# Kernel tuning notes

Hardware: AMD Instinct MI355X
Metric: run time of the kernel (lower is better)

Reference implementation:

```python
import jax, jax.numpy as jnp
import numpy as np
import math

# l values of the spherical harmonics (mul=1 each), matching init_kwargs l=[0..8]
LS = [0, 1, 2, 3, 4, 5, 6, 7, 8]
LMAX = max(LS)
SQRT2 = math.sqrt(2.0)


def _legendre_coeffs(l, m):
    """Coefficients of the associated-Legendre polynomial used by e3nn:
    P_{l,m}(z,y) = norm * y^m * d^{l+m}/dz^{l+m} (z^2-1)^l,
    norm = sqrt((2l+1)/(4pi) (l-m)!/(l+m)!) / (2^l l!).
    Returns list of (power_of_z, float_coeff); the y^m factor is applied by the caller.
    Matches sympy expansion in _sympy_legendre/_poly_legendre exactly.
    """
    n = l + m
    norm = math.sqrt((2 * l + 1) / (4 * math.pi) * math.factorial(l - m) / math.factorial(l + m))
    norm /= (2.0 ** l) * math.factorial(l)
    out = []
    for k in range(l + 1):
        p = 2 * k  # (z^2-1)^l = sum_k C(l,k) (-1)^{l-k} z^{2k}
        if p >= n:
            c = math.comb(l, k) * ((-1) ** (l - k)) * (math.factorial(p) // math.factorial(p - n))
            out.append((p - n, norm * c))
    return out


def _powers(x, pmax):
    pows = [jnp.ones_like(x)]
    for _ in range(pmax):
        pows.append(pows[-1] * x)
    return pows  # pows[p] = x**p


def _legendre_eval(z, y):
    """Equivalent of the fx Legendre graph: [..., sum(2l+1)] with P_{l,|m|} repeated for m=-l..l."""
    zp = _powers(z, 2 * LMAX)
    yp = _powers(y, LMAX)
    cols = []
    for l in LS:
        legs = []
        for m in range(l + 1):
            acc = None
            for pw, c in _legendre_coeffs(l, m):
                term = c * zp[pw]
                acc = term if acc is None else acc + term
            legs.append(acc * yp[m])
        for m in range(-l, l + 1):
            cols.append(legs[abs(m)])
    return jnp.stack(cols, axis=-1)


def _sh_alpha(alpha):
    """spherical_harmonics_alpha for l=LMAX: [..., 2*LMAX+1]."""
    a = alpha[..., None]
    m = jnp.arange(1, LMAX + 1, dtype=alpha.dtype)
    cos = jnp.cos(m * a)           # m = 1..LMAX
    sin = jnp.sin(m[::-1] * a)     # m = LMAX..1
    return jnp.concatenate([SQRT2 * sin, jnp.ones_like(a), SQRT2 * cos], axis=-1)


def _mul_m_lm(x_m, x_lm):
    """Segment-wise multiply of [..., sum(2l+1)] by centered slices of [..., 2*LMAX+1]."""
    out = []
    i = 0
    for l in LS:
        d = 2 * l + 1
        out.append(x_lm[..., i:i + d] * x_m[..., LMAX - l:LMAX + l + 1])
        i += d
    return jnp.concatenate(out, axis=-1)


def setup_inputs() -> dict:
    key = jax.random.key(0)
    k1, k2 = jax.random.split(key)
    n = 1_048_576
    alpha = jax.random.uniform(k1, (n,), jnp.float32, 0.0, 2.0 * math.pi)
    beta = jax.random.uniform(k2, (n,), jnp.float32, 0.0, math.pi)
    return {"alpha": alpha, "beta": beta}


def reference(alpha, beta):
    # forward: y=cos(beta), z=sin(beta); Legendre graph placeholders are (z, y),
    # so the polynomial variable is cos(beta) and the y=sqrt(1-z^2) factor is sin(beta).
    z = jnp.cos(beta)
    y = jnp.sin(beta)
    sha = _sh_alpha(alpha.reshape(-1))                      # [N, 2*LMAX+1]
    shy = _legendre_eval(z.reshape(-1), y.reshape(-1))      # [N, sum(2l+1)]
    out = _mul_m_lm(sha, shy)
    return out.reshape(alpha.shape + (shy.shape[-1],))
```

## Files before the change

kernel.cpp:

```cpp
#include <hip/hip_runtime.h>

#define LMAXV 8
#define NCOL 81
#define ROWB 324
#define BLOCKSZ 64
#define BCHUNK (BLOCKSZ * ROWB)
#define NU4 (BCHUNK / 16)

typedef unsigned int u32x4 __attribute__((ext_vector_type(4)));

struct LMCoef { float c[5]; int T; int par; };

constexpr double cfact(int n) { double r = 1.0; for (int i = 2; i <= n; ++i) r *= (double)i; return r; }
constexpr double ccomb(int n, int k) { return cfact(n) / (cfact(k) * cfact(n - k)); }
constexpr double csqrt_(double x) { double g = x > 1.0 ? x : 1.0; for (int i = 0; i < 200; ++i) g = 0.5 * (g + x / g); return g; }
constexpr double CPI_ = 3.14159265358979323846;

constexpr LMCoef make_lm(int l, int m) {
  LMCoef r{{0.f, 0.f, 0.f, 0.f, 0.f}, 0, 0};
  const int n = l + m;
  const double norm = csqrt_((double)(2 * l + 1) / (4.0 * CPI_) * cfact(l - m) / cfact(l + m))
                      / ((double)(1 << l) * cfact(l));
  r.par = (l - m) & 1;
  r.T = (l - m) / 2 + 1;
  for (int j = 0; j < r.T; ++j) {
    const int p = 2 * j + r.par + n;
    const int k = p / 2;
    const double c = ccomb(l, k) * (((l - k) & 1) ? -1.0 : 1.0) * (cfact(p) / cfact(p - n));
    r.c[j] = (float)(norm * c);
  }
  return r;
}

constexpr LMCoef G_LM[45] = {
  make_lm(0,0),
  make_lm(1,0), make_lm(1,1),
  make_lm(2,0), make_lm(2,1), make_lm(2,2),
  make_lm(3,0), make_lm(3,1), make_lm(3,2), make_lm(3,3),
  make_lm(4,0), make_lm(4,1), make_lm(4,2), make_lm(4,3), make_lm(4,4),
  make_lm(5,0), make_lm(5,1), make_lm(5,2), make_lm(5,3), make_lm(5,4), make_lm(5,5),
  make_lm(6,0), make_lm(6,1), make_lm(6,2), make_lm(6,3), make_lm(6,4), make_lm(6,5), make_lm(6,6),
  make_lm(7,0), make_lm(7,1), make_lm(7,2), make_lm(7,3), make_lm(7,4), make_lm(7,5), make_lm(7,6), make_lm(7,7),
  make_lm(8,0), make_lm(8,1), make_lm(8,2), make_lm(8,3), make_lm(8,4), make_lm(8,5), make_lm(8,6), make_lm(8,7), make_lm(8,8)
};

__global__ __launch_bounds__(BLOCKSZ) void sh_ab_kernel(
    const float* __restrict__ alpha,
    const float* __restrict__ beta,
    float* __restrict__ out, int n)
{
  __shared__ u32x4 ldsbuf[NU4];
  float* lds = (float*)ldsbuf;

  const int tid = blockIdx.x * BLOCKSZ + threadIdx.x;

  float a = 0.f, b = 0.f;
  if (tid < n) {
    a = alpha[tid];
    b = beta[tid];
  }
  float sa, ca, sb, cbeta;
  __sincosf(a, &sa, &ca);
  __sincosf(b, &sb, &cbeta);
  const float z = cbeta, y = sb;
  const float z2 = z * z;

  float S[LMAXV + 1], C[LMAXV + 1];
  S[1] = 1.41421356237309505f * sa;
  C[1] = 1.41421356237309505f * ca;
#pragma unroll
  for (int m = 2; m <= LMAXV; ++m) {
    C[m] = C[m - 1] * ca - S[m - 1] * sa;
    S[m] = S[m - 1] * ca + C[m - 1] * sa;
  }

  float YM[LMAXV + 1], ZYM[LMAXV + 1];
  YM[0] = 1.f;
#pragma unroll
  for (int m = 1; m <= LMAXV; ++m) YM[m] = YM[m - 1] * y;
#pragma unroll
  for (int m = 0; m <= LMAXV; ++m) ZYM[m] = z * YM[m];

  float* myrow = lds + threadIdx.x * NCOL;

#pragma unroll
  for (int l = 0; l <= LMAXV; ++l) {
    float leg[LMAXV + 1];
#pragma unroll
    for (int mm = 0; mm <= l; ++mm) {
      const int idx = l * (l + 1) / 2 + mm;
      float v = 0.f;
#pragma unroll
      for (int j = 4; j >= 0; --j) {
        if (j < G_LM[idx].T) v = v * z2 + G_LM[idx].c[j];
      }
      leg[mm] = v * (G_LM[idx].par ? ZYM[mm] : YM[mm]);
    }
    const int colbase = l * l;
#pragma unroll
    for (int j = 0; j < l; ++j) {
      myrow[colbase + j] = leg[l - j] * S[l - j];
    }
    myrow[colbase + l] = leg[0];
#pragma unroll
    for (int j = 1; j <= l; ++j) {
      myrow[colbase + l + j] = leg[j] * C[j];
    }
  }

  __syncthreads();

  const u32x4* lsrc = (const u32x4*)lds;
  u32x4* gdst = (u32x4*)((char*)out + (size_t)blockIdx.x * BCHUNK);

  if (blockIdx.x != gridDim.x - 1) {
#pragma unroll
    for (int k = 0; k < 20; ++k) {
      const int o = threadIdx.x + (k << 6);
      gdst[o] = lsrc[o];
    }
    if (threadIdx.x < 16) {
      const int o = threadIdx.x + 1280;
      gdst[o] = lsrc[o];
    }
  } else {
    const long limitBytes = (long)n * ROWB - (long)blockIdx.x * BCHUNK;
    for (int o = threadIdx.x; o < NU4; o += BLOCKSZ) {
      if ((long)o * 16 < limitBytes) gdst[o] = lsrc[o];
    }
  }
}

extern "C" void kernel_launch(void* const* d_in, const int* in_sizes, int n_in,
                              void* d_out, int out_size, void* d_ws, size_t ws_size,
                              hipStream_t stream) {
  const float* alpha = (const float*)d_in[0];
  const float* beta  = (const float*)d_in[1];
  float* out = (float*)d_out;
  const int n = in_sizes[0];
  const int grid = (n + BLOCKSZ - 1) / BLOCKSZ;
  hipLaunchKernelGGL(sh_ab_kernel, dim3(grid), dim3(BLOCKSZ), 0, stream,
                     alpha, beta, out, n);
}
```

Before: 347.1 us.

## Process four tiles per block with double-buffered LDS and nontemporal stores

Each 64-thread block now handles four consecutive 64-point tiles, alternating between two LDS buffers and prefetching the next tile's alpha/beta while computing the current one. The __syncthreads is replaced by an explicit lgkmcnt wait, which is enough only because the block is a single wavefront. Output copies use nontemporal 16-byte stores in groups of four. This cuts the block count and aims to overlap the global stores with the next tile's compute, at the cost of twice the LDS per block, which may lower occupancy.

```diff
diff --git a/kernel.cpp b/kernel.cpp
--- a/kernel.cpp
+++ b/kernel.cpp
@@ -4,8 +4,9 @@
 #define NCOL 81
 #define ROWB 324
 #define BLOCKSZ 64
-#define BCHUNK (BLOCKSZ * ROWB)
-#define NU4 (BCHUNK / 16)
+#define TILES 4
+#define TILEB (BLOCKSZ * ROWB)
+#define NU4T (TILEB / 16)
 
 typedef unsigned int u32x4 __attribute__((ext_vector_type(4)));
 
@@ -44,21 +45,8 @@
   make_lm(8,0), make_lm(8,1), make_lm(8,2), make_lm(8,3), make_lm(8,4), make_lm(8,5), make_lm(8,6), make_lm(8,7), make_lm(8,8)
 };
 
-__global__ __launch_bounds__(BLOCKSZ) void sh_ab_kernel(
-    const float* __restrict__ alpha,
-    const float* __restrict__ beta,
-    float* __restrict__ out, int n)
-{
-  __shared__ u32x4 ldsbuf[NU4];
-  float* lds = (float*)ldsbuf;
-
-  const int tid = blockIdx.x * BLOCKSZ + threadIdx.x;
-
-  float a = 0.f, b = 0.f;
-  if (tid < n) {
-    a = alpha[tid];
-    b = beta[tid];
-  }
+__device__ __forceinline__ void compute_tile(float* __restrict__ buf, int lane,
+                                             float a, float b) {
   float sa, ca, sb, cbeta;
   __sincosf(a, &sa, &ca);
   __sincosf(b, &sb, &cbeta);
@@ -81,7 +69,7 @@
 #pragma unroll
   for (int m = 0; m <= LMAXV; ++m) ZYM[m] = z * YM[m];
 
-  float* myrow = lds + threadIdx.x * NCOL;
+  float* myrow = buf + lane * NCOL;
 
 #pragma unroll
   for (int l = 0; l <= LMAXV; ++l) {
@@ -98,35 +86,71 @@
     }
     const int colbase = l * l;
 #pragma unroll
-    for (int j = 0; j < l; ++j) {
-      myrow[colbase + j] = leg[l - j] * S[l - j];
-    }
+    for (int j = 0; j < l; ++j) myrow[colbase + j] = leg[l - j] * S[l - j];
     myrow[colbase + l] = leg[0];
 #pragma unroll
-    for (int j = 1; j <= l; ++j) {
-      myrow[colbase + l + j] = leg[j] * C[j];
-    }
+    for (int j = 1; j <= l; ++j) myrow[colbase + l + j] = leg[j] * C[j];
+  }
+}
+
+__global__ __launch_bounds__(BLOCKSZ) void sh_ab_kernel(
+    const float* __restrict__ alpha,
+    const float* __restrict__ beta,
+    float* __restrict__ out, int n)
+{
+  __shared__ u32x4 bufA[NU4T];
+  __shared__ u32x4 bufB[NU4T];
+
+  const int lane = threadIdx.x;
+  const long p0 = (long)blockIdx.x * (BLOCKSZ * TILES);
+
+  float a = 0.f, b = 0.f;
+  {
+    const long i = p0 + lane;
+    if (i < n) { a = alpha[i]; b = beta[i]; }
   }
 
-  __syncthreads();
+#pragma unroll
+  for (int t = 0; t < TILES; ++t) {
+    float* buf = (t & 1) ? (float*)bufB : (float*)bufA;
+    const float at = a, bt = b;
 
-  const u32x4* lsrc = (const u32x4*)lds;
-  u32x4* gdst = (u32x4*)((char*)out + (size_t)blockIdx.x * BCHUNK);
+    if (t + 1 < TILES) {
+      const long i = p0 + (long)(t + 1) * BLOCKSZ + lane;
+      a = 0.f; b = 0.f;
+      if (i < n) { a = alpha[i]; b = beta[i]; }
+    }
 
-  if (blockIdx.x != gridDim.x - 1) {
+    compute_tile(buf, lane, at, bt);
+
+    asm volatile("s_waitcnt lgkmcnt(0)" ::: "memory");
+
+    const long tbyte = (p0 + (long)t * BLOCKSZ) * ROWB;
+    const long rem = (long)n * ROWB - tbyte;
+    if (rem <= 0) break;
+    const u32x4* ls = (const u32x4*)buf;
+    u32x4* gd = (u32x4*)((char*)out + tbyte);
+
+    if (rem >= TILEB) {
 #pragma unroll
-    for (int k = 0; k < 20; ++k) {
-      const int o = threadIdx.x + (k << 6);
-      gdst[o] = lsrc[o];
-    }
-    if (threadIdx.x < 16) {
-      const int o = threadIdx.x + 1280;
-      gdst[o] = lsrc[o];
-    }
-  } else {
-    const long limitBytes = (long)n * ROWB - (long)blockIdx.x * BCHUNK;
-    for (int o = threadIdx.x; o < NU4; o += BLOCKSZ) {
-      if ((long)o * 16 < limitBytes) gdst[o] = lsrc[o];
+      for (int g = 0; g < 5; ++g) {
+        u32x4 v0 = ls[lane + (g * 4 + 0) * 64];
+        u32x4 v1 = ls[lane + (g * 4 + 1) * 64];
+        u32x4 v2 = ls[lane + (g * 4 + 2) * 64];
+        u32x4 v3 = ls[lane + (g * 4 + 3) * 64];
+        __builtin_nontemporal_store(v0, &gd[lane + (g * 4 + 0) * 64]);
+        __builtin_nontemporal_store(v1, &gd[lane + (g * 4 + 1) * 64]);
+        __builtin_nontemporal_store(v2, &gd[lane + (g * 4 + 2) * 64]);
+        __builtin_nontemporal_store(v3, &gd[lane + (g * 4 + 3) * 64]);
+      }
+      if (lane < 16) {
+        u32x4 v = ls[1280 + lane];
+        __builtin_nontemporal_store(v, &gd[1280 + lane]);
+      }
+    } else {
+      for (int o = lane; o < NU4T; o += BLOCKSZ) {
+        if ((long)o * 16 < rem) gd[o] = ls[o];
+      }
     }
   }
 }
@@ -138,7 +162,8 @@
   const float* beta  = (const float*)d_in[1];
   float* out = (float*)d_out;
   const int n = in_sizes[0];
-  const int grid = (n + BLOCKSZ - 1) / BLOCKSZ;
+  const int ptsPerBlock = BLOCKSZ * TILES;
+  const int grid = (n + ptsPerBlock - 1) / ptsPerBlock;
   hipLaunchKernelGGL(sh_ab_kernel, dim3(grid), dim3(BLOCKSZ), 0, stream,
                      alpha, beta, out, n);
 }
```

Result: no change. 343.9 us (-0.9%).
